# Optimization experiments

Hardware: AMD Instinct MI355X
Metric: run time of the kernel (lower is better)

The kernel has to match this reference:

```python
import math
import jax, jax.numpy as jnp
import numpy as np

jax.config.update("jax_enable_x64", True)  # torch hash math is int64

L = 16
F = 2
T = 524288
PRIMES = (1, 2654435761, 805459861)
N_MIN = 16
N_MAX = 2048
_b = math.exp((math.log(N_MAX) - math.log(N_MIN)) / (L - 1))
RESOLUTIONS = [math.floor(N_MIN * _b ** i) for i in range(L)]
# corner index bits: bit2 -> x offset, bit1 -> y, bit0 -> z (matches torch buffer)
OFFSETS = jnp.array([[0, 0, 0], [0, 0, 1], [0, 1, 0], [0, 1, 1],
                     [1, 0, 0], [1, 0, 1], [1, 1, 0], [1, 1, 1]], dtype=jnp.int64)


def setup_inputs() -> dict:
    key = jax.random.key(0)
    k1, k2 = jax.random.split(key)
    x = jax.random.uniform(k1, (2097152, 3), dtype=jnp.float32)  # coords in [0,1)
    embeddings = jax.random.uniform(k2, (L, T, F), minval=-1e-4, maxval=1e-4,
                                    dtype=jnp.float32)
    return {"x": x, "embeddings": embeddings}


def _encode(x, embeddings):
    feats = []
    for i, res in enumerate(RESOLUTIONS):
        xs = x * res                               # [N,3]
        xf = xs.astype(jnp.int64)                  # trunc == floor for nonneg
        w = xs - xf.astype(x.dtype)                # [N,3] trilinear weights
        fx, fy, fz = w[:, 0:1], w[:, 1:2], w[:, 2:3]  # [N,1] each
        c = xf[:, None, :] + OFFSETS[None, :, :]   # [N,8,3]
        h = ((c[..., 0] * PRIMES[0])
             ^ (c[..., 1] * PRIMES[1])
             ^ (c[..., 2] * PRIMES[2])) % T        # [N,8]
        corners = embeddings[i][h]                 # [N,8,F] gather
        c00 = corners[:, 0] * (1 - fx) + corners[:, 4] * fx
        c01 = corners[:, 1] * (1 - fx) + corners[:, 5] * fx
        c10 = corners[:, 2] * (1 - fx) + corners[:, 6] * fx
        c11 = corners[:, 3] * (1 - fx) + corners[:, 7] * fx
        c0 = c00 * (1 - fy) + c10 * fy
        c1 = c01 * (1 - fy) + c11 * fy
        feats.append(c0 * (1 - fz) + c1 * fz)      # [N,F]
    return jnp.concatenate(feats, axis=-1)         # [N, L*F]


def reference(x, embeddings):
    return _encode(x, embeddings)
```

## Files before the change

### kernel.cpp

```cpp
#include <hip/hip_runtime.h>
#include <cmath>

#define L_LEVELS 16
#define T_SIZE 524288u
#define T_MASK (T_SIZE - 1u)
#define P1 2654435761u
#define P2 805459861u

struct ResArr { int r[L_LEVELS]; };

__device__ __forceinline__ float2 encode_point(
    float px, float py, float pz, float rf,
    const float2* __restrict__ E, const float4* __restrict__ E4)
{
    const float sx = px * rf, sy = py * rf, sz = pz * rf;
    const int ix = (int)sx, iy = (int)sy, iz = (int)sz;
    const float fx = sx - (float)ix;
    const float fy = sy - (float)iy;
    const float fz = sz - (float)iz;

    const unsigned hx0 = (unsigned)ix,      hx1 = hx0 + 1u;
    const unsigned hy0 = (unsigned)iy * P1, hy1 = hy0 + P1;
    const unsigned hz0 = (unsigned)iz * P2, hz1 = hz0 + P2;
    const unsigned diffx = hx0 ^ hx1;

    const unsigned h0 = (hx0 ^ hy0 ^ hz0) & T_MASK;
    const unsigned h1 = (hx0 ^ hy0 ^ hz1) & T_MASK;
    const unsigned h2 = (hx0 ^ hy1 ^ hz0) & T_MASK;
    const unsigned h3 = (hx0 ^ hy1 ^ hz1) & T_MASK;

    float2 c0v, c1v, c2v, c3v, c4v, c5v, c6v, c7v;

    if (diffx == 1u) {
        const float4 v0 = E4[h0 >> 1];
        const float4 v1 = E4[h1 >> 1];
        const float4 v2 = E4[h2 >> 1];
        const float4 v3 = E4[h3 >> 1];
        const bool o0 = (h0 & 1u), o1 = (h1 & 1u), o2 = (h2 & 1u), o3 = (h3 & 1u);
        c0v = o0 ? make_float2(v0.z, v0.w) : make_float2(v0.x, v0.y);
        c1v = o1 ? make_float2(v1.z, v1.w) : make_float2(v1.x, v1.y);
        c2v = o2 ? make_float2(v2.z, v2.w) : make_float2(v2.x, v2.y);
        c3v = o3 ? make_float2(v3.z, v3.w) : make_float2(v3.x, v3.y);
        c4v = o0 ? make_float2(v0.x, v0.y) : make_float2(v0.z, v0.w);
        c5v = o1 ? make_float2(v1.x, v1.y) : make_float2(v1.z, v1.w);
        c6v = o2 ? make_float2(v2.x, v2.y) : make_float2(v2.z, v2.w);
        c7v = o3 ? make_float2(v3.x, v3.y) : make_float2(v3.z, v3.w);
    } else {
        c0v = E[h0];
        c1v = E[h1];
        c2v = E[h2];
        c3v = E[h3];
        c4v = E[h0 ^ diffx];
        c5v = E[h1 ^ diffx];
        c6v = E[h2 ^ diffx];
        c7v = E[h3 ^ diffx];
    }

    const float gx = 1.0f - fx, gy = 1.0f - fy, gz = 1.0f - fz;
    const float c00x = c0v.x * gx + c4v.x * fx;
    const float c00y = c0v.y * gx + c4v.y * fx;
    const float c01x = c1v.x * gx + c5v.x * fx;
    const float c01y = c1v.y * gx + c5v.y * fx;
    const float c10x = c2v.x * gx + c6v.x * fx;
    const float c10y = c2v.y * gx + c6v.y * fx;
    const float c11x = c3v.x * gx + c7v.x * fx;
    const float c11y = c3v.y * gx + c7v.y * fx;

    const float a0x = c00x * gy + c10x * fy;
    const float a0y = c00y * gy + c10y * fy;
    const float a1x = c01x * gy + c11x * fy;
    const float a1y = c01y * gy + c11y * fy;

    return make_float2(a0x * gz + a1x * fz, a0y * gz + a1y * fz);
}

__global__ __launch_bounds__(256) void enc_level_kernel(
    const float* __restrict__ x,
    const float* __restrict__ emb,
    float2* __restrict__ ws,
    ResArr res, int npts)
{
    __shared__ float xsh[768];
    const int tid   = threadIdx.x;
    const int level = blockIdx.y;
    const int pbase = blockIdx.x * 256;

    if (pbase + 256 <= npts) {
        if (tid < 192)
            ((float4*)xsh)[tid] = ((const float4*)(x + (size_t)pbase * 3))[tid];
    } else {
        const int nfl = npts * 3 - pbase * 3;
        for (int i = tid; i < nfl; i += 256) xsh[i] = x[(size_t)pbase * 3 + i];
    }
    __syncthreads();

    const int p = pbase + tid;
    if (p >= npts) return;

    const float rf = (float)res.r[level];
    const float2* __restrict__ E  = (const float2*)emb + (size_t)level * T_SIZE;
    const float4* __restrict__ E4 = (const float4*)E;

    const float2 r = encode_point(xsh[tid * 3 + 0], xsh[tid * 3 + 1],
                                  xsh[tid * 3 + 2], rf, E, E4);
    ws[(size_t)level * npts + p] = r;
}

__global__ __launch_bounds__(256) void transpose_tile_kernel(
    const float2* __restrict__ ws, float4* __restrict__ out4, int npts)
{
    __shared__ float2 tile[256 * 17];
    const int t     = threadIdx.x;
    const int pbase = blockIdx.x * 256;

    if (pbase + 256 <= npts) {
        #pragma unroll
        for (int l = 0; l < L_LEVELS; ++l)
            tile[t * 17 + l] = ws[(size_t)l * npts + pbase + t];
        __syncthreads();

        #pragma unroll
        for (int i = 0; i < 8; ++i) {
            const int jl = i * 256 + t;
            const int pl = jl >> 3;
            const int k  = jl & 7;
            const float2 a = tile[pl * 17 + 2 * k];
            const float2 b = tile[pl * 17 + 2 * k + 1];
            out4[(size_t)pbase * 8 + jl] = make_float4(a.x, a.y, b.x, b.y);
        }
    } else {
        const int p = pbase + t;
        if (p < npts) {
            #pragma unroll
            for (int l = 0; l < L_LEVELS; ++l)
                tile[t * 17 + l] = ws[(size_t)l * npts + p];
        }
        __syncthreads();
        const int npts_loc = npts - pbase;
        for (int i = 0; i < 8; ++i) {
            const int jl = i * 256 + t;
            const int pl = jl >> 3;
            const int k  = jl & 7;
            if (pl < npts_loc) {
                const float2 a = tile[pl * 17 + 2 * k];
                const float2 b = tile[pl * 17 + 2 * k + 1];
                out4[(size_t)pbase * 8 + jl] = make_float4(a.x, a.y, b.x, b.y);
            }
        }
    }
}

__global__ __launch_bounds__(256) void hash_enc_fallback(
    const float* __restrict__ x,
    const float* __restrict__ emb,
    float* __restrict__ out,
    ResArr res, int npts)
{
    __shared__ float xsh[48];
    const int tid = threadIdx.x;
    const int blockPointBase = blockIdx.x * 16;
    if (tid < 48) xsh[tid] = x[(size_t)blockPointBase * 3 + tid];
    __syncthreads();

    const int lp    = tid >> 4;
    const int level = tid & 15;
    const int p     = blockPointBase + lp;
    if (p >= npts) return;

    const float rf = (float)res.r[level];
    const float2* __restrict__ E  = (const float2*)emb + (size_t)level * T_SIZE;
    const float4* __restrict__ E4 = (const float4*)E;

    const float2 r = encode_point(xsh[lp * 3 + 0], xsh[lp * 3 + 1],
                                  xsh[lp * 3 + 2], rf, E, E4);
    ((float2*)out)[(size_t)p * 16 + level] = r;
}

extern "C" void kernel_launch(void* const* d_in, const int* in_sizes, int n_in,
                              void* d_out, int out_size, void* d_ws, size_t ws_size,
                              hipStream_t stream) {
    const float* x   = (const float*)d_in[0];
    const float* emb = (const float*)d_in[1];

    ResArr res;
    const double b = exp((log(2048.0) - log(16.0)) / 15.0);
    for (int i = 0; i < L_LEVELS; ++i)
        res.r[i] = (int)floor(16.0 * pow(b, (double)i));

    const int npts = in_sizes[0] / 3;
    const size_t ws_needed = (size_t)npts * L_LEVELS * sizeof(float2);

    if (ws_size >= ws_needed) {
        float2* ws = (float2*)d_ws;
        const int pblocks = (npts + 255) / 256;
        hipLaunchKernelGGL(enc_level_kernel, dim3(pblocks, L_LEVELS), dim3(256),
                           0, stream, x, emb, ws, res, npts);
        hipLaunchKernelGGL(transpose_tile_kernel, dim3(pblocks), dim3(256),
                           0, stream, ws, (float4*)d_out, npts);
    } else {
        const int blocks = (npts + 15) / 16;
        hipLaunchKernelGGL(hash_enc_fallback, dim3(blocks), dim3(256),
                           0, stream, x, emb, (float*)d_out, res, npts);
    }
}
```

Baseline: 1.175 ms.

## Spatially bin-sort points before per-level encoding to improve gather locality

Adds a counting sort of the input points into a 32^3 spatial grid (histogram, single-block scan, atomic scatter), runs the per-level hash-grid encode on the sorted points, and un-permutes the results during the transpose into the output. Neighbouring points then touch nearby grid cells, so coarse-level embedding gathers should hit cache more often. The cost is extra passes over the points, global atomics, a serial scan, and scattered output writes in the transpose.

```diff
diff --git a/kernel.cpp b/kernel.cpp
--- a/kernel.cpp
+++ b/kernel.cpp
@@ -6,6 +6,10 @@
 #define T_MASK (T_SIZE - 1u)
 #define P1 2654435761u
 #define P2 805459861u
+
+#define NBB   5
+#define NB1   (1 << NBB)
+#define NBINS (1 << (3 * NBB))
 
 struct ResArr { int r[L_LEVELS]; };
 
@@ -74,6 +78,130 @@
     return make_float2(a0x * gz + a1x * fz, a0y * gz + a1y * fz);
 }
 
+__device__ __forceinline__ unsigned bin_key(float px, float py, float pz)
+{
+    int bx = (int)(px * (float)NB1); bx = bx > NB1 - 1 ? NB1 - 1 : bx;
+    int by = (int)(py * (float)NB1); by = by > NB1 - 1 ? NB1 - 1 : by;
+    int bz = (int)(pz * (float)NB1); bz = bz > NB1 - 1 ? NB1 - 1 : bz;
+    return (((unsigned)bz << NBB | (unsigned)by) << NBB) | (unsigned)bx;
+}
+
+__global__ __launch_bounds__(256) void hist_kernel(
+    const float* __restrict__ x, unsigned* __restrict__ hist, int npts)
+{
+    int i = blockIdx.x * 256 + threadIdx.x;
+    const int stride = gridDim.x * 256;
+    for (; i < npts; i += stride) {
+        const size_t b = (size_t)i * 3;
+        atomicAdd(&hist[bin_key(x[b], x[b + 1], x[b + 2])], 1u);
+    }
+}
+
+__global__ __launch_bounds__(1024) void scan_kernel(unsigned* __restrict__ hist)
+{
+    __shared__ unsigned part[1024];
+    const int t = threadIdx.x;
+    unsigned v[NBINS / 1024];
+    unsigned s = 0;
+    #pragma unroll
+    for (int j = 0; j < NBINS / 1024; ++j) { v[j] = hist[t * (NBINS / 1024) + j]; s += v[j]; }
+    part[t] = s;
+    __syncthreads();
+    if (t == 0) {
+        unsigned run = 0;
+        for (int i = 0; i < 1024; ++i) { const unsigned tmp = part[i]; part[i] = run; run += tmp; }
+    }
+    __syncthreads();
+    unsigned run = part[t];
+    #pragma unroll
+    for (int j = 0; j < NBINS / 1024; ++j) { const unsigned tmp = v[j]; hist[t * (NBINS / 1024) + j] = run; run += tmp; }
+}
+
+__global__ __launch_bounds__(256) void scatter_kernel(
+    const float* __restrict__ x, unsigned* __restrict__ cursor,
+    float4* __restrict__ xs4, int npts)
+{
+    __shared__ float xsh[768];
+    const int tid = threadIdx.x, pbase = blockIdx.x * 256;
+    if (pbase + 256 <= npts) {
+        if (tid < 192)
+            ((float4*)xsh)[tid] = ((const float4*)(x + (size_t)pbase * 3))[tid];
+    } else {
+        const int nfl = npts * 3 - pbase * 3;
+        for (int i = tid; i < nfl; i += 256) xsh[i] = x[(size_t)pbase * 3 + i];
+    }
+    __syncthreads();
+    const int p = pbase + tid;
+    if (p >= npts) return;
+    const float px = xsh[tid * 3], py = xsh[tid * 3 + 1], pz = xsh[tid * 3 + 2];
+    const unsigned dest = atomicAdd(&cursor[bin_key(px, py, pz)], 1u);
+    xs4[dest] = make_float4(px, py, pz, __uint_as_float((unsigned)p));
+}
+
+__global__ __launch_bounds__(256) void enc_level_sorted(
+    const float4* __restrict__ xs4,
+    const float* __restrict__ emb,
+    float2* __restrict__ ws,
+    ResArr res, int npts)
+{
+    const int level = blockIdx.y;
+    const int p = blockIdx.x * 256 + threadIdx.x;
+    if (p >= npts) return;
+    const float4 q = xs4[p];
+    const float rf = (float)res.r[level];
+    const float2* __restrict__ E  = (const float2*)emb + (size_t)level * T_SIZE;
+    const float4* __restrict__ E4 = (const float4*)E;
+    ws[(size_t)level * npts + p] = encode_point(q.x, q.y, q.z, rf, E, E4);
+}
+
+__global__ __launch_bounds__(256) void transpose_unperm_kernel(
+    const float2* __restrict__ ws, const float4* __restrict__ xs4,
+    float4* __restrict__ out4, int npts)
+{
+    __shared__ float2 tile[256 * 17];
+    __shared__ unsigned pidx[256];
+    const int t = threadIdx.x, pbase = blockIdx.x * 256;
+
+    if (pbase + 256 <= npts) {
+        #pragma unroll
+        for (int l = 0; l < L_LEVELS; ++l)
+            tile[t * 17 + l] = ws[(size_t)l * npts + pbase + t];
+        pidx[t] = __float_as_uint(((const float*)xs4)[4 * (size_t)(pbase + t) + 3]);
+        __syncthreads();
+
+        #pragma unroll
+        for (int pass = 0; pass < 4; ++pass) {
+            const int pl = pass * 64 + (t >> 2);
+            const int qd = t & 3;
+            const size_t prow = (size_t)pidx[pl];
+            #pragma unroll
+            for (int half = 0; half < 2; ++half) {
+                const int chunk = half * 4 + qd;
+                const float2 a = tile[pl * 17 + 2 * chunk];
+                const float2 b = tile[pl * 17 + 2 * chunk + 1];
+                out4[prow * 8 + chunk] = make_float4(a.x, a.y, b.x, b.y);
+            }
+        }
+    } else {
+        const int p = pbase + t;
+        if (p < npts) {
+            #pragma unroll
+            for (int l = 0; l < L_LEVELS; ++l)
+                tile[t * 17 + l] = ws[(size_t)l * npts + p];
+            pidx[t] = __float_as_uint(((const float*)xs4)[4 * (size_t)p + 3]);
+        }
+        __syncthreads();
+        if (p < npts) {
+            const size_t prow = (size_t)pidx[t];
+            for (int k = 0; k < 8; ++k) {
+                const float2 a = tile[t * 17 + 2 * k];
+                const float2 b = tile[t * 17 + 2 * k + 1];
+                out4[prow * 8 + k] = make_float4(a.x, a.y, b.x, b.y);
+            }
+        }
+    }
+}
+
 __global__ __launch_bounds__(256) void enc_level_kernel(
     const float* __restrict__ x,
     const float* __restrict__ emb,
@@ -118,7 +246,6 @@
         for (int l = 0; l < L_LEVELS; ++l)
             tile[t * 17 + l] = ws[(size_t)l * npts + pbase + t];
         __syncthreads();
-
         #pragma unroll
         for (int i = 0; i < 8; ++i) {
             const int jl = i * 256 + t;
@@ -188,11 +315,30 @@
         res.r[i] = (int)floor(16.0 * pow(b, (double)i));
 
     const int npts = in_sizes[0] / 3;
-    const size_t ws_needed = (size_t)npts * L_LEVELS * sizeof(float2);
-
-    if (ws_size >= ws_needed) {
+    const int pblocks = (npts + 255) / 256;
+
+    const size_t ws2_bytes  = (size_t)npts * L_LEVELS * sizeof(float2);
+    const size_t xs4_bytes  = (size_t)npts * sizeof(float4);
+    const size_t hist_bytes = (size_t)NBINS * sizeof(unsigned);
+    const size_t need_sorted = ws2_bytes + xs4_bytes + hist_bytes;
+
+    if (ws_size >= need_sorted) {
+        float2*   ws2  = (float2*)d_ws;
+        float4*   xs4  = (float4*)((char*)d_ws + ws2_bytes);
+        unsigned* hist = (unsigned*)((char*)d_ws + ws2_bytes + xs4_bytes);
+
+        hipMemsetAsync(hist, 0, hist_bytes, stream);
+        hipLaunchKernelGGL(hist_kernel, dim3(2048), dim3(256), 0, stream,
+                           x, hist, npts);
+        hipLaunchKernelGGL(scan_kernel, dim3(1), dim3(1024), 0, stream, hist);
+        hipLaunchKernelGGL(scatter_kernel, dim3(pblocks), dim3(256), 0, stream,
+                           x, hist, xs4, npts);
+        hipLaunchKernelGGL(enc_level_sorted, dim3(pblocks, L_LEVELS), dim3(256),
+                           0, stream, xs4, emb, ws2, res, npts);
+        hipLaunchKernelGGL(transpose_unperm_kernel, dim3(pblocks), dim3(256),
+                           0, stream, ws2, xs4, (float4*)d_out, npts);
+    } else if (ws_size >= ws2_bytes) {
         float2* ws = (float2*)d_ws;
-        const int pblocks = (npts + 255) / 256;
         hipLaunchKernelGGL(enc_level_kernel, dim3(pblocks, L_LEVELS), dim3(256),
                            0, stream, x, emb, ws, res, npts);
         hipLaunchKernelGGL(transpose_tile_kernel, dim3(pblocks), dim3(256),
```

After: 1.152 ms. About the same (-2.0%).
